# Performance work log

Measured on AMD Instinct MI355X. Metric: run time of the kernel, lower is better.

The kernel has to match this reference:

```python
import jax, jax.numpy as jnp
import numpy as np

B, T, D, H, G = 256, 1024, 32, 64, 4 * 64  # batch, seq, input, hidden, gates


def setup_inputs() -> dict:
    key = jax.random.key(0)
    ks = jax.random.split(key, 12)
    s = 1.0 / np.sqrt(H)  # PyTorch LSTM default init scale
    return {
        "x": jax.random.normal(ks[0], (B, T, D), dtype=jnp.float32),
        "w_ih_l0": jax.random.normal(ks[1], (G, D), dtype=jnp.float32) * s,
        "w_hh_l0": jax.random.normal(ks[2], (G, H), dtype=jnp.float32) * s,
        "b_ih_l0": jax.random.normal(ks[3], (G,), dtype=jnp.float32) * s,
        "b_hh_l0": jax.random.normal(ks[4], (G,), dtype=jnp.float32) * s,
        "w_ih_l1": jax.random.normal(ks[5], (G, H), dtype=jnp.float32) * s,
        "w_hh_l1": jax.random.normal(ks[6], (G, H), dtype=jnp.float32) * s,
        "b_ih_l1": jax.random.normal(ks[7], (G,), dtype=jnp.float32) * s,
        "b_hh_l1": jax.random.normal(ks[8], (G,), dtype=jnp.float32) * s,
        "w_fc": jax.random.normal(ks[9], (1, H), dtype=jnp.float32) * s,
        "b_fc": jax.random.normal(ks[10], (1,), dtype=jnp.float32) * s,
    }


def _lstm_layer(x, w_ih, w_hh, b_ih, b_hh):
    """x: [B, T, Din] -> h_seq [B, T, H]. PyTorch gate order (i, f, g, o)."""
    # Precompute input contribution for all timesteps in one GEMM.
    gx = jnp.einsum('btd,gd->btg', x, w_ih) + b_ih + b_hh  # [B, T, 4H]
    gx = jnp.swapaxes(gx, 0, 1)  # [T, B, 4H] for scan over time
    h0 = jnp.zeros((x.shape[0], H), dtype=x.dtype)
    c0 = jnp.zeros((x.shape[0], H), dtype=x.dtype)

    def step(carry, g_t):
        h, c = carry
        g = g_t + h @ w_hh.T  # [B, 4H]
        i, f, gg, o = jnp.split(g, 4, axis=-1)
        i = jax.nn.sigmoid(i)
        f = jax.nn.sigmoid(f)
        gg = jnp.tanh(gg)
        o = jax.nn.sigmoid(o)
        c = f * c + i * gg
        h = o * jnp.tanh(c)
        return (h, c), h

    _, h_seq = jax.lax.scan(step, (h0, c0), gx)  # h_seq: [T, B, H]
    return jnp.swapaxes(h_seq, 0, 1)  # [B, T, H]


def reference(x, w_ih_l0, w_hh_l0, b_ih_l0, b_hh_l0,
              w_ih_l1, w_hh_l1, b_ih_l1, b_hh_l1, w_fc, b_fc):
    h1 = _lstm_layer(x, w_ih_l0, w_hh_l0, b_ih_l0, b_hh_l0)
    h2 = _lstm_layer(h1, w_ih_l1, w_hh_l1, b_ih_l1, b_hh_l1)
    last = h2[:, -1, :]  # [B, H]
    logits = last @ w_fc.T + b_fc  # [B, 1]
    return jax.nn.sigmoid(logits)
```

## Files before the change

### kernel.cpp

```cpp
#include <hip/hip_runtime.h>

#define TT 1024
#define DD 32
#define HH 64

typedef __fp16 h2v __attribute__((ext_vector_type(2)));
typedef _Float16 f16x8 __attribute__((ext_vector_type(8)));
typedef float f32x4 __attribute__((ext_vector_type(4)));

struct __attribute__((aligned(16))) H4 { h2v p[4]; };
struct __attribute__((aligned(8)))  GX2 { h2v a, b; };

__device__ __forceinline__ h2v pk(float a, float b) {
    return __builtin_amdgcn_cvt_pkrtz(a, b);
}
__device__ __forceinline__ float fsig(float x) {
    float e = __builtin_amdgcn_exp2f(-1.4426950408889634f * x);
    return __builtin_amdgcn_rcpf(1.0f + e);
}
__device__ __forceinline__ float ftanh(float x) {
    float e = __builtin_amdgcn_exp2f(2.885390081777927f * x);
    return 1.0f - 2.0f * __builtin_amdgcn_rcpf(1.0f + e);
}
__device__ __forceinline__ float pick4(f32x4 c, bool s0, bool s1) {
    float lo = s0 ? c[1] : c[0];
    float hi = s0 ? c[3] : c[2];
    return s1 ? hi : lo;
}
__device__ __forceinline__ f16x8 load_afrag(const float* p) {
    float4 f0 = *(const float4*)p;
    float4 f1 = *(const float4*)(p + 4);
    H4 t;
    t.p[0] = pk(f0.x, f0.y); t.p[1] = pk(f0.z, f0.w);
    t.p[2] = pk(f1.x, f1.y); t.p[3] = pk(f1.z, f1.w);
    return __builtin_bit_cast(f16x8, t);
}

#define MFMA16(A, B, C) __builtin_amdgcn_mfma_f32_16x16x32_f16(A, B, C, 0, 0, 0)

__global__ __launch_bounds__(256) void gx_precompute(
    const float* __restrict__ x, const float* __restrict__ w_ih_l0,
    const float* __restrict__ b_ih_l0, const float* __restrict__ b_hh_l0,
    __fp16* __restrict__ gx)
{
    const int blk = blockIdx.x;
    const int b   = blk >> 4;
    const int tq  = blk & 15;
    const int tid = threadIdx.x;
    const int q   = tid & 3;
    const int j   = tid >> 2;
    const int g   = q * 64 + j;

    __shared__ __attribute__((aligned(16))) h2v xlds[512];

    h2v wk[16];
    {
        const float4* wp = (const float4*)(w_ih_l0 + g * DD);
        #pragma unroll
        for (int i = 0; i < 8; ++i) {
            float4 f = wp[i];
            wk[2*i]   = pk(f.x, f.y);
            wk[2*i+1] = pk(f.z, f.w);
        }
    }
    const float bias = b_ih_l0[g] + b_hh_l0[g];

    const float* xb = x + (size_t)b * (TT*DD) + tq * 64 * DD;
    __fp16* gxo = gx + ((size_t)b * TT + tq * 64) * 256 + tid;

    #pragma unroll
    for (int sc = 0; sc < 2; ++sc) {
        __syncthreads();
        {
            float4 f = *(const float4*)(xb + sc * 1024 + tid * 4);
            xlds[tid*2]   = pk(f.x, f.y);
            xlds[tid*2+1] = pk(f.z, f.w);
        }
        __syncthreads();
        for (int tl = 0; tl < 32; ++tl) {
            float s0 = 0.f, s1 = 0.f;
            #pragma unroll
            for (int k = 0; k < 8; ++k) s0 = __builtin_amdgcn_fdot2(wk[k],   xlds[tl*16 + k],     s0, false);
            #pragma unroll
            for (int k = 0; k < 8; ++k) s1 = __builtin_amdgcn_fdot2(wk[8+k], xlds[tl*16 + 8 + k], s1, false);
            gxo[(sc*32 + tl) * 256] = (__fp16)(s0 + s1 + bias);
        }
    }
}

__global__ __launch_bounds__(512) void lstm2_mfma(
    const float* __restrict__ w_hh_l0,
    const float* __restrict__ w_ih_l1, const float* __restrict__ w_hh_l1,
    const float* __restrict__ b_ih_l1, const float* __restrict__ b_hh_l1,
    const float* __restrict__ w_fc,   const float* __restrict__ b_fc,
    const __fp16* __restrict__ gx,
    float* __restrict__ out)
{
    const int b    = blockIdx.x;
    const int tid  = threadIdx.x;
    const int wave = tid >> 6;
    const int lane = tid & 63;
    const bool isL1 = wave < 4;
    const int w    = isL1 ? wave : (wave - 4);
    const int colg = lane & 15;
    const int quad = lane >> 4;
    const int j_act = 16*w + quad*4 + (lane & 3);

    __shared__ __attribute__((aligned(16))) __fp16 h1s[2][HH];
    __shared__ __attribute__((aligned(16))) __fp16 h2s[2][HH];
    if (tid < HH) {
        h1s[0][tid] = (__fp16)0.f; h1s[1][tid] = (__fp16)0.f;
        h2s[0][tid] = (__fp16)0.f; h2s[1][tid] = (__fp16)0.f;
    }

    f16x8 Aih[8], Ahh[8];
    float bias0 = 0.f, bias1 = 0.f, bias2 = 0.f, bias3 = 0.f;
    if (isL1) {
        #pragma unroll
        for (int q = 0; q < 4; ++q)
            #pragma unroll
            for (int kh = 0; kh < 2; ++kh)
                Ahh[q*2+kh] = load_afrag(w_hh_l0 + (size_t)(q*64 + 16*w + colg)*HH + kh*32 + quad*8);
    } else {
        #pragma unroll
        for (int q = 0; q < 4; ++q)
            #pragma unroll
            for (int kh = 0; kh < 2; ++kh) {
                Aih[q*2+kh] = load_afrag(w_ih_l1 + (size_t)(q*64 + 16*w + colg)*HH + kh*32 + quad*8);
                Ahh[q*2+kh] = load_afrag(w_hh_l1 + (size_t)(q*64 + 16*w + colg)*HH + kh*32 + quad*8);
            }
        bias0 = b_ih_l1[0*64 + j_act] + b_hh_l1[0*64 + j_act];
        bias1 = b_ih_l1[1*64 + j_act] + b_hh_l1[1*64 + j_act];
        bias2 = b_ih_l1[2*64 + j_act] + b_hh_l1[2*64 + j_act];
        bias3 = b_ih_l1[3*64 + j_act] + b_hh_l1[3*64 + j_act];
    }

    const __fp16* gxp = gx + ((size_t)b << 18) + j_act * 4;
    GX2 gq = {};
    if (isL1) gq = *(const GX2*)gxp;

    const bool s0 = (lane & 1) != 0;
    const bool s1 = (lane & 2) != 0;
    float c = 0.0f;

    __syncthreads();

    for (int t = 0; t <= TT; ++t) {
        const int prev = (t + 1) & 1;
        const int cur  = t & 1;
        if (isL1) {
            if (t < TT) {
                const int tn = (t + 1 < TT) ? (t + 1) : t;
                GX2 gn = *(const GX2*)(gxp + ((size_t)tn << 8));

                const __fp16* hp = &h1s[prev][0];
                f16x8 Blo = *(const f16x8*)(hp + quad*8);
                f16x8 Bhi = *(const f16x8*)(hp + 32 + quad*8);

                f32x4 Z = {0.f, 0.f, 0.f, 0.f};
                f32x4 C0 = Z, C1 = Z, C2 = Z, C3 = Z;
                C0 = MFMA16(Ahh[0], Blo, C0); C0 = MFMA16(Ahh[1], Bhi, C0);
                C1 = MFMA16(Ahh[2], Blo, C1); C1 = MFMA16(Ahh[3], Bhi, C1);
                C2 = MFMA16(Ahh[4], Blo, C2); C2 = MFMA16(Ahh[5], Bhi, C2);
                C3 = MFMA16(Ahh[6], Blo, C3); C3 = MFMA16(Ahh[7], Bhi, C3);

                float Si = pick4(C0, s0, s1) + (float)gq.a[0];
                float Sf = pick4(C1, s0, s1) + (float)gq.a[1];
                float Sg = pick4(C2, s0, s1) + (float)gq.b[0];
                float So = pick4(C3, s0, s1) + (float)gq.b[1];

                float ii = fsig(Si), ff = fsig(Sf), oo = fsig(So);
                float gg = ftanh(Sg);
                c = ff * c + ii * gg;
                float hv = oo * ftanh(c);
                if ((lane & 12) == 0) h1s[cur][j_act] = (__fp16)hv;
                gq = gn;
            }
        } else {
            if (t > 0) {
                const __fp16* hp1 = &h1s[prev][0];
                const __fp16* hp2 = &h2s[prev][0];
                f16x8 B1lo = *(const f16x8*)(hp1 + quad*8);
                f16x8 B1hi = *(const f16x8*)(hp1 + 32 + quad*8);
                f16x8 B2lo = *(const f16x8*)(hp2 + quad*8);
                f16x8 B2hi = *(const f16x8*)(hp2 + 32 + quad*8);

                f32x4 Z = {0.f, 0.f, 0.f, 0.f};
                f32x4 C0 = Z, C1 = Z, C2 = Z, C3 = Z;
                C0 = MFMA16(Aih[0], B1lo, C0); C0 = MFMA16(Aih[1], B1hi, C0);
                C0 = MFMA16(Ahh[0], B2lo, C0); C0 = MFMA16(Ahh[1], B2hi, C0);
                C1 = MFMA16(Aih[2], B1lo, C1); C1 = MFMA16(Aih[3], B1hi, C1);
                C1 = MFMA16(Ahh[2], B2lo, C1); C1 = MFMA16(Ahh[3], B2hi, C1);
                C2 = MFMA16(Aih[4], B1lo, C2); C2 = MFMA16(Aih[5], B1hi, C2);
                C2 = MFMA16(Ahh[4], B2lo, C2); C2 = MFMA16(Ahh[5], B2hi, C2);
                C3 = MFMA16(Aih[6], B1lo, C3); C3 = MFMA16(Aih[7], B1hi, C3);
                C3 = MFMA16(Ahh[6], B2lo, C3); C3 = MFMA16(Ahh[7], B2hi, C3);

                float Si = pick4(C0, s0, s1) + bias0;
                float Sf = pick4(C1, s0, s1) + bias1;
                float Sg = pick4(C2, s0, s1) + bias2;
                float So = pick4(C3, s0, s1) + bias3;

                float ii = fsig(Si), ff = fsig(Sf), oo = fsig(So);
                float gg = ftanh(Sg);
                c = ff * c + ii * gg;
                float hv = oo * ftanh(c);
                if ((lane & 12) == 0) h2s[cur][j_act] = (__fp16)hv;
            }
        }
        __syncthreads();
    }

    if (tid < HH) {
        float v = (float)h2s[0][tid] * w_fc[tid];
        #pragma unroll
        for (int off = 32; off > 0; off >>= 1) v += __shfl_down(v, off);
        if (tid == 0) out[b] = fsig(v + b_fc[0]);
    }
}

extern "C" void kernel_launch(void* const* d_in, const int* in_sizes, int n_in,
                              void* d_out, int out_size, void* d_ws, size_t ws_size,
                              hipStream_t stream) {
    __fp16* gx = (__fp16*)d_ws;
    gx_precompute<<<dim3(256 * 16), dim3(256), 0, stream>>>(
        (const float*)d_in[0], (const float*)d_in[1],
        (const float*)d_in[3], (const float*)d_in[4], gx);
    lstm2_mfma<<<dim3(256), dim3(512), 0, stream>>>(
        (const float*)d_in[2],
        (const float*)d_in[5], (const float*)d_in[6],
        (const float*)d_in[7], (const float*)d_in[8],
        (const float*)d_in[9], (const float*)d_in[10],
        gx, (float*)d_out);
}
```

Before: 556.5 us.

## Fuse input projection into recurrence and batch four sequences per block

Drops the separate gx precompute kernel and its fp16 workspace round-trip. The layer-0 input projection becomes an extra MFMA over x, which one wave streams into LDS with prefetch. Each block now handles four batch elements, filling four MFMA B columns instead of one, so the grid shrinks from 256 to 64 blocks. This removes HBM traffic and a launch, and uses the MFMA width better. The cost is far fewer blocks on a many-CU GPU and one wave doing extra x-loading work on the critical step.

```diff
diff --git a/kernel.cpp b/kernel.cpp
--- a/kernel.cpp
+++ b/kernel.cpp
@@ -9,7 +9,6 @@
 typedef float f32x4 __attribute__((ext_vector_type(4)));
 
 struct __attribute__((aligned(16))) H4 { h2v p[4]; };
-struct __attribute__((aligned(8)))  GX2 { h2v a, b; };
 
 __device__ __forceinline__ h2v pk(float a, float b) {
     return __builtin_amdgcn_cvt_pkrtz(a, b);
@@ -35,201 +34,180 @@
     t.p[2] = pk(f1.x, f1.y); t.p[3] = pk(f1.z, f1.w);
     return __builtin_bit_cast(f16x8, t);
 }
-
 #define MFMA16(A, B, C) __builtin_amdgcn_mfma_f32_16x16x32_f16(A, B, C, 0, 0, 0)
 
-__global__ __launch_bounds__(256) void gx_precompute(
-    const float* __restrict__ x, const float* __restrict__ w_ih_l0,
+__global__ __launch_bounds__(512) void lstm2_b4(
+    const float* __restrict__ x,
+    const float* __restrict__ w_ih_l0, const float* __restrict__ w_hh_l0,
     const float* __restrict__ b_ih_l0, const float* __restrict__ b_hh_l0,
-    __fp16* __restrict__ gx)
-{
-    const int blk = blockIdx.x;
-    const int b   = blk >> 4;
-    const int tq  = blk & 15;
-    const int tid = threadIdx.x;
-    const int q   = tid & 3;
-    const int j   = tid >> 2;
-    const int g   = q * 64 + j;
-
-    __shared__ __attribute__((aligned(16))) h2v xlds[512];
-
-    h2v wk[16];
-    {
-        const float4* wp = (const float4*)(w_ih_l0 + g * DD);
-        #pragma unroll
-        for (int i = 0; i < 8; ++i) {
-            float4 f = wp[i];
-            wk[2*i]   = pk(f.x, f.y);
-            wk[2*i+1] = pk(f.z, f.w);
-        }
-    }
-    const float bias = b_ih_l0[g] + b_hh_l0[g];
-
-    const float* xb = x + (size_t)b * (TT*DD) + tq * 64 * DD;
-    __fp16* gxo = gx + ((size_t)b * TT + tq * 64) * 256 + tid;
-
-    #pragma unroll
-    for (int sc = 0; sc < 2; ++sc) {
-        __syncthreads();
-        {
-            float4 f = *(const float4*)(xb + sc * 1024 + tid * 4);
-            xlds[tid*2]   = pk(f.x, f.y);
-            xlds[tid*2+1] = pk(f.z, f.w);
-        }
-        __syncthreads();
-        for (int tl = 0; tl < 32; ++tl) {
-            float s0 = 0.f, s1 = 0.f;
-            #pragma unroll
-            for (int k = 0; k < 8; ++k) s0 = __builtin_amdgcn_fdot2(wk[k],   xlds[tl*16 + k],     s0, false);
-            #pragma unroll
-            for (int k = 0; k < 8; ++k) s1 = __builtin_amdgcn_fdot2(wk[8+k], xlds[tl*16 + 8 + k], s1, false);
-            gxo[(sc*32 + tl) * 256] = (__fp16)(s0 + s1 + bias);
-        }
-    }
-}
-
-__global__ __launch_bounds__(512) void lstm2_mfma(
-    const float* __restrict__ w_hh_l0,
     const float* __restrict__ w_ih_l1, const float* __restrict__ w_hh_l1,
     const float* __restrict__ b_ih_l1, const float* __restrict__ b_hh_l1,
     const float* __restrict__ w_fc,   const float* __restrict__ b_fc,
-    const __fp16* __restrict__ gx,
     float* __restrict__ out)
 {
-    const int b    = blockIdx.x;
+    const int bbase = blockIdx.x * 4;
     const int tid  = threadIdx.x;
     const int wave = tid >> 6;
     const int lane = tid & 63;
     const bool isL1 = wave < 4;
-    const int w    = isL1 ? wave : (wave - 4);
-    const int colg = lane & 15;
+    const int js   = wave & 3;
     const int quad = lane >> 4;
-    const int j_act = 16*w + quad*4 + (lane & 3);
-
-    __shared__ __attribute__((aligned(16))) __fp16 h1s[2][HH];
-    __shared__ __attribute__((aligned(16))) __fp16 h2s[2][HH];
-    if (tid < HH) {
-        h1s[0][tid] = (__fp16)0.f; h1s[1][tid] = (__fp16)0.f;
-        h2s[0][tid] = (__fp16)0.f; h2s[1][tid] = (__fp16)0.f;
-    }
-
-    f16x8 Aih[8], Ahh[8];
-    float bias0 = 0.f, bias1 = 0.f, bias2 = 0.f, bias3 = 0.f;
+    const int bb   = lane & 3;
+    const int rsel = (lane >> 2) & 3;
+    const int jj   = js*16 + quad*4 + rsel;
+    const int mrow = lane & 15;
+
+    __shared__ __attribute__((aligned(16))) __fp16 buf[1280];
+
+    {
+        int* bi = (int*)buf;
+        bi[tid] = 0;
+        if (tid < 128) bi[512 + tid] = 0;
+    }
+
+    f16x8 A[16];
+    float bs0, bs1, bs2, bs3;
     if (isL1) {
         #pragma unroll
-        for (int q = 0; q < 4; ++q)
-            #pragma unroll
-            for (int kh = 0; kh < 2; ++kh)
-                Ahh[q*2+kh] = load_afrag(w_hh_l0 + (size_t)(q*64 + 16*w + colg)*HH + kh*32 + quad*8);
+        for (int q = 0; q < 4; ++q) {
+            const int g = q*64 + js*16 + mrow;
+            A[q*3 + 0] = load_afrag(w_ih_l0 + (size_t)g*DD + quad*8);
+            A[q*3 + 1] = load_afrag(w_hh_l0 + (size_t)g*HH + quad*8);
+            A[q*3 + 2] = load_afrag(w_hh_l0 + (size_t)g*HH + 32 + quad*8);
+        }
+        bs0 = b_ih_l0[0*64 + jj] + b_hh_l0[0*64 + jj];
+        bs1 = b_ih_l0[1*64 + jj] + b_hh_l0[1*64 + jj];
+        bs2 = b_ih_l0[2*64 + jj] + b_hh_l0[2*64 + jj];
+        bs3 = b_ih_l0[3*64 + jj] + b_hh_l0[3*64 + jj];
     } else {
         #pragma unroll
-        for (int q = 0; q < 4; ++q)
-            #pragma unroll
-            for (int kh = 0; kh < 2; ++kh) {
-                Aih[q*2+kh] = load_afrag(w_ih_l1 + (size_t)(q*64 + 16*w + colg)*HH + kh*32 + quad*8);
-                Ahh[q*2+kh] = load_afrag(w_hh_l1 + (size_t)(q*64 + 16*w + colg)*HH + kh*32 + quad*8);
-            }
-        bias0 = b_ih_l1[0*64 + j_act] + b_hh_l1[0*64 + j_act];
-        bias1 = b_ih_l1[1*64 + j_act] + b_hh_l1[1*64 + j_act];
-        bias2 = b_ih_l1[2*64 + j_act] + b_hh_l1[2*64 + j_act];
-        bias3 = b_ih_l1[3*64 + j_act] + b_hh_l1[3*64 + j_act];
-    }
-
-    const __fp16* gxp = gx + ((size_t)b << 18) + j_act * 4;
-    GX2 gq = {};
-    if (isL1) gq = *(const GX2*)gxp;
-
-    const bool s0 = (lane & 1) != 0;
-    const bool s1 = (lane & 2) != 0;
-    float c = 0.0f;
+        for (int q = 0; q < 4; ++q) {
+            const int g = q*64 + js*16 + mrow;
+            A[q*4 + 0] = load_afrag(w_ih_l1 + (size_t)g*HH + quad*8);
+            A[q*4 + 1] = load_afrag(w_ih_l1 + (size_t)g*HH + 32 + quad*8);
+            A[q*4 + 2] = load_afrag(w_hh_l1 + (size_t)g*HH + quad*8);
+            A[q*4 + 3] = load_afrag(w_hh_l1 + (size_t)g*HH + 32 + quad*8);
+        }
+        bs0 = b_ih_l1[0*64 + jj] + b_hh_l1[0*64 + jj];
+        bs1 = b_ih_l1[1*64 + jj] + b_hh_l1[1*64 + jj];
+        bs2 = b_ih_l1[2*64 + jj] + b_hh_l1[2*64 + jj];
+        bs3 = b_ih_l1[3*64 + jj] + b_hh_l1[3*64 + jj];
+    }
+
+    const int roff = (bb*4 + quad)*8;
+    const int cw   = (isL1 ? 1 : 3) + (jj >> 5);
+    const int woff = ((cw*4 + bb)*4 + ((jj & 31) >> 3))*8 + (jj & 7);
+
+    const float* xg = x + (size_t)(bbase + (lane >> 4)) * (TT*DD) + (lane & 15)*2;
+    const int sdw = ((lane >> 4)*4 + ((lane & 15) >> 2))*4 + ((lane & 15) & 3);
+    float2 xv1 = {0.f, 0.f}, xv2 = {0.f, 0.f};
 
     __syncthreads();
+    if (wave == 7) {
+        float2 v0 = *(const float2*)xg;
+        ((int*)buf)[sdw] = __builtin_bit_cast(int, pk(v0.x, v0.y));
+        xv1 = *(const float2*)(xg + DD);
+        xv2 = *(const float2*)(xg + 2*DD);
+    }
+    __syncthreads();
+
+    const bool s0 = (rsel & 1) != 0;
+    const bool s1 = (rsel & 2) != 0;
+    float cst = 0.0f;
 
     for (int t = 0; t <= TT; ++t) {
-        const int prev = (t + 1) & 1;
-        const int cur  = t & 1;
+        const int p = t & 1;
+        const __fp16* bc = buf + p*640;
+        __fp16* bn = buf + (p ^ 1)*640;
         if (isL1) {
             if (t < TT) {
-                const int tn = (t + 1 < TT) ? (t + 1) : t;
-                GX2 gn = *(const GX2*)(gxp + ((size_t)tn << 8));
-
-                const __fp16* hp = &h1s[prev][0];
-                f16x8 Blo = *(const f16x8*)(hp + quad*8);
-                f16x8 Bhi = *(const f16x8*)(hp + 32 + quad*8);
+                f16x8 B0 = *(const f16x8*)(bc + 0*128 + roff);
+                f16x8 B1 = *(const f16x8*)(bc + 1*128 + roff);
+                f16x8 B2 = *(const f16x8*)(bc + 2*128 + roff);
 
                 f32x4 Z = {0.f, 0.f, 0.f, 0.f};
                 f32x4 C0 = Z, C1 = Z, C2 = Z, C3 = Z;
-                C0 = MFMA16(Ahh[0], Blo, C0); C0 = MFMA16(Ahh[1], Bhi, C0);
-                C1 = MFMA16(Ahh[2], Blo, C1); C1 = MFMA16(Ahh[3], Bhi, C1);
-                C2 = MFMA16(Ahh[4], Blo, C2); C2 = MFMA16(Ahh[5], Bhi, C2);
-                C3 = MFMA16(Ahh[6], Blo, C3); C3 = MFMA16(Ahh[7], Bhi, C3);
-
-                float Si = pick4(C0, s0, s1) + (float)gq.a[0];
-                float Sf = pick4(C1, s0, s1) + (float)gq.a[1];
-                float Sg = pick4(C2, s0, s1) + (float)gq.b[0];
-                float So = pick4(C3, s0, s1) + (float)gq.b[1];
+                C0 = MFMA16(A[0], B0, C0); C0 = MFMA16(A[1],  B1, C0); C0 = MFMA16(A[2],  B2, C0);
+                C1 = MFMA16(A[3], B0, C1); C1 = MFMA16(A[4],  B1, C1); C1 = MFMA16(A[5],  B2, C1);
+                C2 = MFMA16(A[6], B0, C2); C2 = MFMA16(A[7],  B1, C2); C2 = MFMA16(A[8],  B2, C2);
+                C3 = MFMA16(A[9], B0, C3); C3 = MFMA16(A[10], B1, C3); C3 = MFMA16(A[11], B2, C3);
+
+                float Si = pick4(C0, s0, s1) + bs0;
+                float Sf = pick4(C1, s0, s1) + bs1;
+                float Sg = pick4(C2, s0, s1) + bs2;
+                float So = pick4(C3, s0, s1) + bs3;
 
                 float ii = fsig(Si), ff = fsig(Sf), oo = fsig(So);
                 float gg = ftanh(Sg);
-                c = ff * c + ii * gg;
-                float hv = oo * ftanh(c);
-                if ((lane & 12) == 0) h1s[cur][j_act] = (__fp16)hv;
-                gq = gn;
+                cst = ff * cst + ii * gg;
+                float hv = oo * ftanh(cst);
+                bn[woff] = (__fp16)hv;
             }
         } else {
+            if (wave == 7 && t < TT) {
+                ((int*)bn)[sdw] = __builtin_bit_cast(int, pk(xv1.x, xv1.y));
+                xv1 = xv2;
+                const int tl = (t + 3 < TT) ? (t + 3) : (TT - 1);
+                xv2 = *(const float2*)(xg + (size_t)tl*DD);
+            }
             if (t > 0) {
-                const __fp16* hp1 = &h1s[prev][0];
-                const __fp16* hp2 = &h2s[prev][0];
-                f16x8 B1lo = *(const f16x8*)(hp1 + quad*8);
-                f16x8 B1hi = *(const f16x8*)(hp1 + 32 + quad*8);
-                f16x8 B2lo = *(const f16x8*)(hp2 + quad*8);
-                f16x8 B2hi = *(const f16x8*)(hp2 + 32 + quad*8);
+                f16x8 B1 = *(const f16x8*)(bc + 1*128 + roff);
+                f16x8 B2 = *(const f16x8*)(bc + 2*128 + roff);
+                f16x8 B3 = *(const f16x8*)(bc + 3*128 + roff);
+                f16x8 B4 = *(const f16x8*)(bc + 4*128 + roff);
 
                 f32x4 Z = {0.f, 0.f, 0.f, 0.f};
                 f32x4 C0 = Z, C1 = Z, C2 = Z, C3 = Z;
-                C0 = MFMA16(Aih[0], B1lo, C0); C0 = MFMA16(Aih[1], B1hi, C0);
-                C0 = MFMA16(Ahh[0], B2lo, C0); C0 = MFMA16(Ahh[1], B2hi, C0);
-                C1 = MFMA16(Aih[2], B1lo, C1); C1 = MFMA16(Aih[3], B1hi, C1);
-                C1 = MFMA16(Ahh[2], B2lo, C1); C1 = MFMA16(Ahh[3], B2hi, C1);
-                C2 = MFMA16(Aih[4], B1lo, C2); C2 = MFMA16(Aih[5], B1hi, C2);
-                C2 = MFMA16(Ahh[4], B2lo, C2); C2 = MFMA16(Ahh[5], B2hi, C2);
-                C3 = MFMA16(Aih[6], B1lo, C3); C3 = MFMA16(Aih[7], B1hi, C3);
-                C3 = MFMA16(Ahh[6], B2lo, C3); C3 = MFMA16(Ahh[7], B2hi, C3);
-
-                float Si = pick4(C0, s0, s1) + bias0;
-                float Sf = pick4(C1, s0, s1) + bias1;
-                float Sg = pick4(C2, s0, s1) + bias2;
-                float So = pick4(C3, s0, s1) + bias3;
+                C0 = MFMA16(A[0],  B1, C0); C0 = MFMA16(A[1],  B2, C0);
+                C0 = MFMA16(A[2],  B3, C0); C0 = MFMA16(A[3],  B4, C0);
+                C1 = MFMA16(A[4],  B1, C1); C1 = MFMA16(A[5],  B2, C1);
+                C1 = MFMA16(A[6],  B3, C1); C1 = MFMA16(A[7],  B4, C1);
+                C2 = MFMA16(A[8],  B1, C2); C2 = MFMA16(A[9],  B2, C2);
+                C2 = MFMA16(A[10], B3, C2); C2 = MFMA16(A[11], B4, C2);
+                C3 = MFMA16(A[12], B1, C3); C3 = MFMA16(A[13], B2, C3);
+                C3 = MFMA16(A[14], B3, C3); C3 = MFMA16(A[15], B4, C3);
+
+                float Si = pick4(C0, s0, s1) + bs0;
+                float Sf = pick4(C1, s0, s1) + bs1;
+                float Sg = pick4(C2, s0, s1) + bs2;
+                float So = pick4(C3, s0, s1) + bs3;
 
                 float ii = fsig(Si), ff = fsig(Sf), oo = fsig(So);
                 float gg = ftanh(Sg);
-                c = ff * c + ii * gg;
-                float hv = oo * ftanh(c);
-                if ((lane & 12) == 0) h2s[cur][j_act] = (__fp16)hv;
+                cst = ff * cst + ii * gg;
+                float hv = oo * ftanh(cst);
+                bn[woff] = (__fp16)hv;
             }
         }
         __syncthreads();
     }
 
-    if (tid < HH) {
-        float v = (float)h2s[0][tid] * w_fc[tid];
+    if (wave == 0) {
+        const int jg = lane >> 2;
+        float s = 0.f;
         #pragma unroll
-        for (int off = 32; off > 0; off >>= 1) v += __shfl_down(v, off);
-        if (tid == 0) out[b] = fsig(v + b_fc[0]);
+        for (int u2 = 0; u2 < 4; ++u2) {
+            const int j = jg*4 + u2;
+            float hval = (float)buf[640 + (((3 + (j >> 5))*4 + bb)*4 + ((j & 31) >> 3))*8 + (j & 7)];
+            s += hval * w_fc[j];
+        }
+        s += __shfl_xor(s, 4);
+        s += __shfl_xor(s, 8);
+        s += __shfl_xor(s, 16);
+        s += __shfl_xor(s, 32);
+        if (lane < 4) out[bbase + lane] = fsig(s + b_fc[0]);
     }
 }
 
 extern "C" void kernel_launch(void* const* d_in, const int* in_sizes, int n_in,
                               void* d_out, int out_size, void* d_ws, size_t ws_size,
                               hipStream_t stream) {
-    __fp16* gx = (__fp16*)d_ws;
-    gx_precompute<<<dim3(256 * 16), dim3(256), 0, stream>>>(
-        (const float*)d_in[0], (const float*)d_in[1],
-        (const float*)d_in[3], (const float*)d_in[4], gx);
-    lstm2_mfma<<<dim3(256), dim3(512), 0, stream>>>(
-        (const float*)d_in[2],
+    lstm2_b4<<<dim3(64), dim3(512), 0, stream>>>(
+        (const float*)d_in[0],
+        (const float*)d_in[1], (const float*)d_in[2],
+        (const float*)d_in[3], (const float*)d_in[4],
         (const float*)d_in[5], (const float*)d_in[6],
         (const float*)d_in[7], (const float*)d_in[8],
         (const float*)d_in[9], (const float*)d_in[10],
-        gx, (float*)d_out);
-}
+        (float*)d_out);
+}
```

After: 545.4 us (median of 3 runs). 2.0% less time.
